# Kernel tuning notes

Measured on AMD Instinct MI355X. Metric: run time of the kernel, lower is better.

## Reference

```python
import jax, jax.numpy as jnp
import numpy as np

B, T, D = 2, 2048, 1024
H, HD = 16, 32
INNER = H * HD
FF = 4 * D
KT, KP = 3, 15


def _layernorm(x, g, b, eps=1e-5):
    mu = jnp.mean(x, axis=-1, keepdims=True)
    var = jnp.var(x, axis=-1, keepdims=True)
    return (x - mu) * jax.lax.rsqrt(var + eps) * g + b


def _causal_dwconv(x, w, b):
    # x: (b,t,d), w: (d,1,k) depthwise kernel; causal left-pad of k-1
    k = w.shape[-1]
    xc = jnp.transpose(x, (0, 2, 1))  # (b,d,t)
    xp = jnp.pad(xc, ((0, 0), (0, 0), (k - 1, 0)))
    y = jax.lax.conv_general_dilated(
        xp, w, window_strides=(1,), padding='VALID',
        feature_group_count=x.shape[-1],
        dimension_numbers=('NCH', 'OIH', 'NCH'))
    return jnp.transpose(y + b[None, :, None], (0, 2, 1))


def _causal_linear_attention(q, k, v, mask):
    # q,k,v: (b,t,h,d); mask: (b,t)
    m = mask[:, :, None, None]
    q = (jax.nn.elu(q) + 1.0) * m
    k = (jax.nn.elu(k) + 1.0) * m
    v = v * m
    kv = jnp.einsum('bthd,bthe->bthde', k, v)
    kv_prefix = jnp.cumsum(kv, axis=1)          # (b,t,h,d,e) large intermediate
    k_prefix = jnp.cumsum(k, axis=1)
    num = jnp.einsum('bthd,bthde->bthe', q, kv_prefix)
    den = jnp.sum(q * k_prefix, axis=-1, keepdims=True)
    return (num / (den + 1e-6)) * m


def setup_inputs() -> dict:
    key = jax.random.key(0)
    ks = jax.random.split(key, 10)
    w = lambda i, shape: jax.random.normal(ks[i], shape, jnp.float32) * 0.02
    return {
        'inputs': jax.random.normal(ks[0], (B, T, D), jnp.float32),
        'mask': jnp.ones((B, T), jnp.float32),
        'ln1_g': jnp.ones((D,), jnp.float32), 'ln1_b': jnp.zeros((D,), jnp.float32),
        'W_in': w(1, (D, D + 3 * INNER)), 'b_in': jnp.zeros((D + 3 * INNER,), jnp.float32),
        'W_c': w(2, (INNER, D)), 'b_c': jnp.zeros((D,), jnp.float32),
        'w_t': w(3, (D, 1, KT)), 'b_t': jnp.zeros((D,), jnp.float32),
        'w_p': w(4, (D, 1, KP)), 'b_p': jnp.zeros((D,), jnp.float32),
        'W_mix': w(5, (3 * D, D)), 'b_mix': jnp.zeros((D,), jnp.float32),
        'ln2_g': jnp.ones((D,), jnp.float32), 'ln2_b': jnp.zeros((D,), jnp.float32),
        'W1': w(6, (D, FF)), 'b1': jnp.zeros((FF,), jnp.float32),
        'W2': w(7, (FF, D)), 'b2': jnp.zeros((D,), jnp.float32),
    }


def reference(inputs, mask, ln1_g, ln1_b, W_in, b_in, W_c, b_c, w_t, b_t,
              w_p, b_p, W_mix, b_mix, ln2_g, ln2_b, W1, b1, W2, b2):
    residual = inputs
    normed = _layernorm(inputs, ln1_g, ln1_b)
    proj = normed @ W_in + b_in
    gate, q, k, v = jnp.split(proj, [D, D + INNER, D + 2 * INNER], axis=-1)
    b, t, _ = inputs.shape
    q = q.reshape(b, t, H, HD)
    k = k.reshape(b, t, H, HD)
    v = v.reshape(b, t, H, HD)
    content = _causal_linear_attention(q, k, v, mask).reshape(b, t, INNER)
    content = content @ W_c + b_c
    temporal = _causal_dwconv(normed, w_t, b_t)
    positional = _causal_dwconv(normed, w_p, b_p)
    mixed = jnp.concatenate((content, temporal, positional), axis=-1) @ W_mix + b_mix
    mask_f = mask[:, :, None]
    out = residual + jax.nn.sigmoid(gate) * mixed  # dropout=0.0 -> identity
    out = out * mask_f
    h = _layernorm(out, ln2_g, ln2_b)
    ffn = jax.nn.gelu(h @ W1 + b1, approximate=False) @ W2 + b2
    out = out + ffn
    return out * mask_f
```

## Files before the change

kernel.cpp:

```cpp
#include <hip/hip_runtime.h>
#include <math.h>

#define BB 2
#define TT 2048
#define DD 1024
#define HH 16
#define INNERD 512
#define FFD 4096
#define NPROJ 2560
#define CATD2 2560
#define MROWS (BB*TT)
#define CHUNK 64
#define NCH (TT/CHUNK)
#define BH 32

typedef __bf16 bf16;
typedef __attribute__((ext_vector_type(8))) __bf16 bf16x8;
typedef __attribute__((ext_vector_type(4))) __bf16 bf16x4;
typedef __attribute__((ext_vector_type(4))) float f32x4;

struct Part4 { void* p0; void* p1; void* p2; void* p3; };

__global__ __launch_bounds__(256) void prep_fused(
    const float* __restrict__ inputs, const float* __restrict__ ln1_g,
    const float* __restrict__ ln1_b, bf16* __restrict__ normed,
    const float* __restrict__ W_in,  bf16* __restrict__ wt_in,
    const float* __restrict__ W_mix, bf16* __restrict__ wt_m0,
    bf16* __restrict__ wt_comb,
    const float* __restrict__ W1,    bf16* __restrict__ wt1,
    const float* __restrict__ W2,    bf16* __restrict__ wt2,
    const float* __restrict__ W_c,   bf16* __restrict__ wc_b,
    const float* __restrict__ b_c,
    const float* __restrict__ b_mix, float* __restrict__ bmix2)
{
    int blk = blockIdx.x, tid = threadIdx.x;
    if (blk < 16) {
        int nl = tid & 63, jg = tid >> 6;
        int n = blk * 64 + nl;
        int j0 = jg * 256;
        float acc = 0.f;
        #pragma unroll 8
        for (int j = 0; j < 256; j++)
            acc = fmaf(b_c[j0 + j], W_mix[(size_t)(j0 + j) * DD + n], acc);
        __shared__ float red[4][64];
        red[jg][nl] = acc;
        __syncthreads();
        if (jg == 0)
            bmix2[n] = b_mix[n] + red[0][nl] + red[1][nl] + red[2][nl] + red[3][nl];
        return;
    }
    if (blk < 528) {
        int id = (blk - 16) * 256 + tid;
        f32x4 v = ((const f32x4*)W_c)[id];
        bf16x4 o;
        #pragma unroll
        for (int q = 0; q < 4; q++) o[q] = (bf16)v[q];
        ((bf16x4*)wc_b)[id] = o;
        return;
    }
    if (blk < 528 + MROWS) {
        int row = blk - 528;
        f32x4 xv = ((const f32x4*)(inputs + (size_t)row * DD))[tid];
        float s = xv[0] + xv[1] + xv[2] + xv[3];
        float s2 = xv[0]*xv[0] + xv[1]*xv[1] + xv[2]*xv[2] + xv[3]*xv[3];
        #pragma unroll
        for (int off = 32; off > 0; off >>= 1) {
            s  += __shfl_xor(s,  off, 64);
            s2 += __shfl_xor(s2, off, 64);
        }
        __shared__ float rs[4], rs2[4];
        int wid = tid >> 6;
        if ((tid & 63) == 0) { rs[wid] = s; rs2[wid] = s2; }
        __syncthreads();
        s  = rs[0] + rs[1] + rs[2] + rs[3];
        s2 = rs2[0] + rs2[1] + rs2[2] + rs2[3];
        float mean = s * (1.0f / DD);
        float var  = s2 * (1.0f / DD) - mean * mean;
        float rstd = rsqrtf(var + 1e-5f);
        f32x4 gv = ((const f32x4*)ln1_g)[tid];
        f32x4 bv = ((const f32x4*)ln1_b)[tid];
        bf16x4 o;
        #pragma unroll
        for (int q = 0; q < 4; q++)
            o[q] = (bf16)((xv[q] - mean) * rstd * gv[q] + bv[q]);
        ((bf16x4*)(normed + (size_t)row * DD))[tid] = o;
        return;
    }
    int tb = blk - (528 + MROWS);
    const float* W; bf16* Wt = nullptr; int Kd, Nd; bool is_mix = false;
    if      (tb < 2560)  {             W = W_in;  Wt = wt_in;  Kd = 1024; Nd = 2560; }
    else if (tb < 5632)  { tb -= 2560; W = W_mix;              Kd = 3072; Nd = 1024; is_mix = true; }
    else if (tb < 9728)  { tb -= 5632; W = W1;    Wt = wt1;    Kd = 1024; Nd = 4096; }
    else                 { tb -= 9728; W = W2;    Wt = wt2;    Kd = 4096; Nd = 1024; }
    int ntx = Nd >> 5;
    int nb = (tb % ntx) * 32, kb = (tb / ntx) * 32;
    int ldW = Kd, kw = kb;
    if (is_mix) {
        if (kb < 1024) { Wt = wt_m0;   ldW = 1024;  kw = kb; }
        else           { Wt = wt_comb; ldW = CATD2; kw = kb - 512; }
    }
    __shared__ float t[32][33];
    int tx = tid & 7, ty = tid >> 3;
    f32x4 v = *(const f32x4*)(W + (size_t)(kb + ty) * Nd + nb + tx * 4);
    #pragma unroll
    for (int q = 0; q < 4; q++) t[ty][tx * 4 + q] = v[q];
    __syncthreads();
    bf16x4 o;
    #pragma unroll
    for (int q = 0; q < 4; q++) o[q] = (bf16)t[tx * 4 + q][ty];
    *(bf16x4*)(Wt + (size_t)(nb + ty) * ldW + kw + tx * 4) = o;
}

template<int EPI>
__global__ __launch_bounds__(256, 4) void gemm_mfma(
    const bf16* __restrict__ A,  int lda,
    const bf16* __restrict__ Bt, int ldb,
    const float* __restrict__ bias,
    bf16* __restrict__ Cb, int ldc,
    int K, Part4 part)
{
    __shared__ bf16 As[128 * 64];
    __shared__ bf16 Bs[128 * 64];
    const int tid  = threadIdx.x;
    const int wave = tid >> 6, lane = tid & 63;
    const int m0 = blockIdx.x * 128, n0 = blockIdx.y * 128;
    const int koff = blockIdx.z * K;
    A  += koff;
    Bt += koff;
    const int wr = wave >> 1, wc = wave & 1;
    const int lrow = lane >> 2;
    const int lcol = (lane & 3) * 8;
    const int fm = lane & 15;
    const int fk = (lane >> 4) * 8;

    f32x4 acc[4][4];
    #pragma unroll
    for (int i = 0; i < 4; i++)
        #pragma unroll
        for (int j = 0; j < 4; j++)
            acc[i][j] = (f32x4){0.f, 0.f, 0.f, 0.f};

    for (int k0 = 0; k0 < K; k0 += 64) {
        #pragma unroll
        for (int r = 0; r < 4; r++) {
            int c  = r * 4 + wave;
            int rc = c >> 1, kh = c & 1;
            const bf16* ga = A  + (size_t)(m0 + rc * 16 + lrow) * lda + k0 + kh * 32 + lcol;
            const bf16* gb = Bt + (size_t)(n0 + rc * 16 + lrow) * ldb + k0 + kh * 32 + lcol;
            __builtin_amdgcn_global_load_lds(
                (const __attribute__((address_space(1))) void*)ga,
                (__attribute__((address_space(3))) void*)(As + c * 512), 16, 0, 0);
            __builtin_amdgcn_global_load_lds(
                (const __attribute__((address_space(1))) void*)gb,
                (__attribute__((address_space(3))) void*)(Bs + c * 512), 16, 0, 0);
        }
        __syncthreads();
        #pragma unroll
        for (int ks = 0; ks < 2; ks++) {
            bf16x8 af[4], bfv[4];
            #pragma unroll
            for (int i = 0; i < 4; i++)
                af[i] = *(const bf16x8*)(As + (wr * 4 + i) * 1024 + ks * 512 + fm * 32 + fk);
            #pragma unroll
            for (int j = 0; j < 4; j++)
                bfv[j] = *(const bf16x8*)(Bs + (wc * 4 + j) * 1024 + ks * 512 + fm * 32 + fk);
            #pragma unroll
            for (int i = 0; i < 4; i++)
                #pragma unroll
                for (int j = 0; j < 4; j++)
                    acc[i][j] = __builtin_amdgcn_mfma_f32_16x16x32_bf16(
                        af[i], bfv[j], acc[i][j], 0, 0, 0);
        }
        __syncthreads();
    }

    void* psel = nullptr;
    if constexpr (EPI == 4) {
        int z = blockIdx.z;
        psel = (z == 0) ? part.p0 : (z == 1) ? part.p1 : (z == 2) ? part.p2 : part.p3;
    }

    #pragma unroll
    for (int i = 0; i < 4; i++) {
        int mbase = m0 + wr * 64 + i * 16 + (lane >> 4) * 4;
        #pragma unroll
        for (int j = 0; j < 4; j++) {
            int col = n0 + wc * 64 + j * 16 + (lane & 15);
            float bv = 0.f;
            if constexpr (EPI == 0 || EPI == 1) bv = bias[col];
            #pragma unroll
            for (int r = 0; r < 4; r++) {
                int row = mbase + r;
                float v = acc[i][j][r] + bv;
                if constexpr (EPI == 0) {
                    Cb[(size_t)row * ldc + col] = (bf16)v;
                } else if constexpr (EPI == 1) {
                    float z2 = v * (1.5957691f + 0.07135502f * v * v);
                    v = v / (1.0f + __expf(-z2));
                    Cb[(size_t)row * ldc + col] = (bf16)v;
                } else {
                    ((bf16*)psel)[(size_t)row * DD + col] = (bf16)v;
                }
            }
        }
    }
}

__global__ __launch_bounds__(256, 4) void gemm_proj2(
    const bf16* __restrict__ normed, const bf16* __restrict__ wt_in,
    const float* __restrict__ bias,  bf16* __restrict__ proj,
    const bf16* __restrict__ wt_m0,  const bf16* __restrict__ wc_b,
    bf16* __restrict__ wt_comb)
{
    __shared__ bf16 As[128 * 64];
    __shared__ bf16 Bs[128 * 64];
    const int tid  = threadIdx.x;
    const int wave = tid >> 6, lane = tid & 63;
    const bool second = (blockIdx.y == 20);
    const bf16* A  = second ? wt_m0 : normed;
    const bf16* Bt = second ? wc_b  : wt_in;
    bf16* Cb       = second ? wt_comb : proj;
    const int m0 = second ? ((blockIdx.x >> 2) * 128) : (blockIdx.x * 128);
    const int n0 = second ? ((blockIdx.x & 3) * 128)  : (blockIdx.y * 128);
    const int wr = wave >> 1, wc = wave & 1;
    const int lrow = lane >> 2;
    const int lcol = (lane & 3) * 8;
    const int fm = lane & 15;
    const int fk = (lane >> 4) * 8;

    f32x4 acc[4][4];
    #pragma unroll
    for (int i = 0; i < 4; i++)
        #pragma unroll
        for (int j = 0; j < 4; j++)
            acc[i][j] = (f32x4){0.f, 0.f, 0.f, 0.f};

    for (int k0 = 0; k0 < DD; k0 += 64) {
        #pragma unroll
        for (int r = 0; r < 4; r++) {
            int c  = r * 4 + wave;
            int rc = c >> 1, kh = c & 1;
            const bf16* ga = A  + (size_t)(m0 + rc * 16 + lrow) * DD + k0 + kh * 32 + lcol;
            const bf16* gb = Bt + (size_t)(n0 + rc * 16 + lrow) * DD + k0 + kh * 32 + lcol;
            __builtin_amdgcn_global_load_lds(
                (const __attribute__((address_space(1))) void*)ga,
                (__attribute__((address_space(3))) void*)(As + c * 512), 16, 0, 0);
            __builtin_amdgcn_global_load_lds(
                (const __attribute__((address_space(1))) void*)gb,
                (__attribute__((address_space(3))) void*)(Bs + c * 512), 16, 0, 0);
        }
        __syncthreads();
        #pragma unroll
        for (int ks = 0; ks < 2; ks++) {
            bf16x8 af[4], bfv[4];
            #pragma unroll
            for (int i = 0; i < 4; i++)
                af[i] = *(const bf16x8*)(As + (wr * 4 + i) * 1024 + ks * 512 + fm * 32 + fk);
            #pragma unroll
            for (int j = 0; j < 4; j++)
                bfv[j] = *(const bf16x8*)(Bs + (wc * 4 + j) * 1024 + ks * 512 + fm * 32 + fk);
            #pragma unroll
            for (int i = 0; i < 4; i++)
                #pragma unroll
                for (int j = 0; j < 4; j++)
                    acc[i][j] = __builtin_amdgcn_mfma_f32_16x16x32_bf16(
                        af[i], bfv[j], acc[i][j], 0, 0, 0);
        }
        __syncthreads();
    }

    #pragma unroll
    for (int i = 0; i < 4; i++) {
        int mbase = m0 + wr * 64 + i * 16 + (lane >> 4) * 4;
        #pragma unroll
        for (int j = 0; j < 4; j++) {
            int col = n0 + wc * 64 + j * 16 + (lane & 15);
            float bv = second ? 0.f : bias[col];
            #pragma unroll
            for (int r = 0; r < 4; r++) {
                int row = mbase + r;
                Cb[(size_t)row * CATD2 + col] = (bf16)(acc[i][j][r] + bv);
            }
        }
    }
}

__global__ __launch_bounds__(256) void epi_mix_ln2(
    const bf16* __restrict__ P0, const bf16* __restrict__ P1,
    const float* __restrict__ bias,
    const bf16* __restrict__ proj, const float* __restrict__ res,
    const float* __restrict__ mask,
    const float* __restrict__ g2, const float* __restrict__ b2v,
    float* __restrict__ out1, bf16* __restrict__ hbuf)
{
    int row = blockIdx.x, tid = threadIdx.x;
    float m = mask[row];
    size_t off = (size_t)row * DD + tid * 4;
    bf16x4 s0 = *(const bf16x4*)(P0 + off);
    bf16x4 s1 = *(const bf16x4*)(P1 + off);
    f32x4 bv = ((const f32x4*)bias)[tid];
    bf16x4 g4 = *(const bf16x4*)(proj + (size_t)row * NPROJ + tid * 4);
    f32x4 rv = ((const f32x4*)(res + (size_t)row * DD))[tid];
    f32x4 v;
    #pragma unroll
    for (int q = 0; q < 4; q++) {
        float sg = 1.0f / (1.0f + __expf(-(float)g4[q]));
        float sv = (float)s0[q] + (float)s1[q] + bv[q];
        v[q] = (rv[q] + sg * sv) * m;
    }
    ((f32x4*)(out1 + (size_t)row * DD))[tid] = v;
    float s = v[0] + v[1] + v[2] + v[3];
    float s2 = v[0]*v[0] + v[1]*v[1] + v[2]*v[2] + v[3]*v[3];
    #pragma unroll
    for (int off2 = 32; off2 > 0; off2 >>= 1) {
        s  += __shfl_xor(s,  off2, 64);
        s2 += __shfl_xor(s2, off2, 64);
    }
    __shared__ float rs[4], rs2[4];
    int wid = tid >> 6;
    if ((tid & 63) == 0) { rs[wid] = s; rs2[wid] = s2; }
    __syncthreads();
    s  = rs[0] + rs[1] + rs[2] + rs[3];
    s2 = rs2[0] + rs2[1] + rs2[2] + rs2[3];
    float mean = s * (1.0f / DD);
    float var  = s2 * (1.0f / DD) - mean * mean;
    float rstd = rsqrtf(var + 1e-5f);
    f32x4 gg = ((const f32x4*)g2)[tid];
    f32x4 bb = ((const f32x4*)b2v)[tid];
    bf16x4 h;
    #pragma unroll
    for (int q = 0; q < 4; q++)
        h[q] = (bf16)((v[q] - mean) * rstd * gg[q] + bb[q]);
    ((bf16x4*)(hbuf + (size_t)row * DD))[tid] = h;
}

__global__ __launch_bounds__(256) void epi_w2(
    float* __restrict__ d_out, const float* __restrict__ out1,
    const bf16* __restrict__ P0, const bf16* __restrict__ P1,
    const bf16* __restrict__ P2, const bf16* __restrict__ P3,
    const float* __restrict__ bias, const float* __restrict__ mask)
{
    int id = blockIdx.x * 256 + threadIdx.x;
    int row = id >> 8;
    float m = mask[row];
    bf16x4 a0 = ((const bf16x4*)P0)[id];
    bf16x4 a1 = ((const bf16x4*)P1)[id];
    bf16x4 a2 = ((const bf16x4*)P2)[id];
    bf16x4 a3 = ((const bf16x4*)P3)[id];
    f32x4 r = ((const f32x4*)out1)[id];
    f32x4 b = ((const f32x4*)bias)[id & 255];
    f32x4 o;
    #pragma unroll
    for (int q = 0; q < 4; q++) {
        float sv = (float)a0[q] + (float)a1[q] + (float)a2[q] + (float)a3[q];
        o[q] = (r[q] + sv + b[q]) * m;
    }
    ((f32x4*)d_out)[id] = o;
}

__device__ __forceinline__ float phi_f(float x) {
    return x > 0.f ? x + 1.f : __expf(x);
}

__global__ __launch_bounds__(256) void mid_fused(
    const bf16* __restrict__ x,
    const float* __restrict__ w_t, const float* __restrict__ b_t,
    const float* __restrict__ w_p, const float* __restrict__ b_p,
    bf16* __restrict__ cat,
    const bf16* __restrict__ proj, const float* __restrict__ mask,
    float* __restrict__ kvsum, float* __restrict__ kssum)
{
    __shared__ float s_ks[2][CHUNK][32], s_vs[2][CHUNK][32];
    int blk = blockIdx.x, tid = threadIdx.x;
    if (blk < 1024) {
        int id = blk * 256 + tid;
        int cg = id & 127, rp = id >> 7;
        int c0 = cg * 8;
        int row0 = rp * 2;
        int t0 = row0 & (TT - 1);
        bf16x8 xw[16];
        #pragma unroll
        for (int j = 0; j < 16; j++) {
            int t = t0 - 14 + j;
            if (t >= 0)
                xw[j] = *(const bf16x8*)(x + (size_t)(row0 - 14 + j) * DD + c0);
            else
                #pragma unroll
                for (int q = 0; q < 8; q++) xw[j][q] = (bf16)0.f;
        }
        float y15[2][8], y3[2][8];
        #pragma unroll
        for (int q = 0; q < 8; q++) {
            float bp = b_p[c0 + q], bt = b_t[c0 + q];
            y15[0][q] = bp; y15[1][q] = bp;
            y3[0][q] = bt;  y3[1][q] = bt;
        }
        #pragma unroll
        for (int i = 0; i < 15; i++) {
            float wp[8];
            #pragma unroll
            for (int q = 0; q < 8; q++) wp[q] = w_p[(c0 + q) * 15 + i];
            #pragma unroll
            for (int rr = 0; rr < 2; rr++)
                #pragma unroll
                for (int q = 0; q < 8; q++)
                    y15[rr][q] = fmaf(wp[q], (float)xw[rr + i][q], y15[rr][q]);
        }
        #pragma unroll
        for (int i = 0; i < 3; i++) {
            float wt[8];
            #pragma unroll
            for (int q = 0; q < 8; q++) wt[q] = w_t[(c0 + q) * 3 + i];
            #pragma unroll
            for (int rr = 0; rr < 2; rr++)
                #pragma unroll
                for (int q = 0; q < 8; q++)
                    y3[rr][q] = fmaf(wt[q], (float)xw[rr + 12 + i][q], y3[rr][q]);
        }
        #pragma unroll
        for (int rr = 0; rr < 2; rr++) {
            bf16x8 o3, o15;
            #pragma unroll
            for (int q = 0; q < 8; q++) { o3[q] = (bf16)y3[rr][q]; o15[q] = (bf16)y15[rr][q]; }
            *(bf16x8*)(cat + (size_t)(row0 + rr) * CATD2 + 512 + c0)  = o3;
            *(bf16x8*)(cat + (size_t)(row0 + rr) * CATD2 + 1536 + c0) = o15;
        }
        return;
    }
    int w = tid >> 6;
    if (w >= 2) return;
    int lane = tid & 63;
    int ci = (blk - 1024) * 2 + w;
    int c  = ci & (NCH - 1);
    int bh = ci >> 5;
    int b  = bh >> 4, hh = bh & (HH - 1);
    float (*ks)[32] = s_ks[w];
    float (*vs)[32] = s_vs[w];
    int row0 = b * TT + c * CHUNK;
    {
        int row = row0 + lane;
        float m = mask[row];
        const bf16* kp = proj + (size_t)row * NPROJ + DD + INNERD + hh * 32;
        const bf16* vp = kp + INNERD;
        #pragma unroll
        for (int s = 0; s < 4; s++) {
            bf16x8 k8 = *(const bf16x8*)(kp + s * 8);
            bf16x8 v8 = *(const bf16x8*)(vp + s * 8);
            #pragma unroll
            for (int q = 0; q < 8; q++) {
                ks[lane][s * 8 + q] = phi_f((float)k8[q]) * m;
                vs[lane][s * 8 + q] = (float)v8[q] * m;
            }
        }
    }
    int e = lane & 31, d0 = (lane >> 5) * 16;
    float kv[16], ksl[16];
    #pragma unroll
    for (int j = 0; j < 16; j++) { kv[j] = 0.f; ksl[j] = 0.f; }
    for (int t = 0; t < CHUNK; t++) {
        float ve = vs[t][e];
        f32x4 kr[4];
        #pragma unroll
        for (int s = 0; s < 4; s++) kr[s] = *(const f32x4*)&ks[t][d0 + s * 4];
        #pragma unroll
        for (int j = 0; j < 16; j++) {
            float kval = kr[j >> 2][j & 3];
            kv[j] = fmaf(kval, ve, kv[j]);
            ksl[j] += kval;
        }
    }
    size_t base = (size_t)ci * 1024;
    #pragma unroll
    for (int j = 0; j < 16; j++)
        kvsum[base + (size_t)(d0 + j) * 32 + e] = kv[j];
    if (e == 0) {
        #pragma unroll
        for (int j = 0; j < 16; j++)
            kssum[ci * 32 + d0 + j] = ksl[j];
    }
}

__global__ __launch_bounds__(256) void attn_prefix(
    const float* __restrict__ kvsum, const float* __restrict__ kssum,
    float* __restrict__ kvpref, float* __restrict__ kspref)
{
    int blk = blockIdx.x, tid = threadIdx.x;
    if (blk < 128) {
        int bh = blk >> 2;
        int de = (blk & 3) * 256 + tid;
        float run = 0.f;
        for (int c = 0; c < NCH; c++) {
            size_t a = (size_t)(bh * NCH + c) * 1024 + de;
            kvpref[a] = run;
            run += kvsum[a];
        }
        return;
    }
    int id = (blk - 128) * 256 + tid;
    int bh = id >> 5, d = id & 31;
    float r = 0.f;
    for (int c = 0; c < NCH; c++) {
        int a = (bh * NCH + c) * 32 + d;
        kspref[a] = r;
        r += kssum[a];
    }
}

__global__ __launch_bounds__(64) void attn_scan(
    const bf16* __restrict__ proj, const float* __restrict__ mask,
    const float* __restrict__ kvpref, const float* __restrict__ kspref,
    bf16* __restrict__ cat)
{
    int blk = blockIdx.x;
    int c  = blk & (NCH - 1);
    int bh = blk >> 5;
    int b  = bh >> 4, hh = bh & (HH - 1);
    int lane = threadIdx.x;
    __shared__ float qs[CHUNK][32], ks[CHUNK][32], vs[CHUNK][32];
    __shared__ float ms[CHUNK];
    int row0 = b * TT + c * CHUNK;
    {
        int row = row0 + lane;
        float m = mask[row];
        ms[lane] = m;
        const bf16* qp = proj + (size_t)row * NPROJ + DD + hh * 32;
        const bf16* kp = qp + INNERD;
        const bf16* vp = kp + INNERD;
        #pragma unroll
        for (int s = 0; s < 4; s++) {
            bf16x8 q8 = *(const bf16x8*)(qp + s * 8);
            bf16x8 k8 = *(const bf16x8*)(kp + s * 8);
            bf16x8 v8 = *(const bf16x8*)(vp + s * 8);
            #pragma unroll
            for (int q = 0; q < 8; q++) {
                qs[lane][s * 8 + q] = phi_f((float)q8[q]) * m;
                ks[lane][s * 8 + q] = phi_f((float)k8[q]) * m;
                vs[lane][s * 8 + q] = (float)v8[q] * m;
            }
        }
    }
    int e = lane & 31, d0 = (lane >> 5) * 16;
    float kv[16], ksl[16];
    size_t base = (size_t)blk * 1024;
    #pragma unroll
    for (int j = 0; j < 16; j++) kv[j] = kvpref[base + (size_t)(d0 + j) * 32 + e];
    #pragma unroll
    for (int j = 0; j < 16; j++) ksl[j] = kspref[blk * 32 + d0 + j];
    __syncthreads();
    for (int t = 0; t < CHUNK; t++) {
        float ve = vs[t][e];
        f32x4 kr[4], qr[4];
        #pragma unroll
        for (int s = 0; s < 4; s++) kr[s] = *(const f32x4*)&ks[t][d0 + s * 4];
        #pragma unroll
        for (int s = 0; s < 4; s++) qr[s] = *(const f32x4*)&qs[t][d0 + s * 4];
        float num0 = 0.f, num1 = 0.f, den0 = 0.f, den1 = 0.f;
        #pragma unroll
        for (int j = 0; j < 16; j++) {
            float kval = kr[j >> 2][j & 3], qval = qr[j >> 2][j & 3];
            kv[j]  = fmaf(kval, ve, kv[j]);
            ksl[j] += kval;
            if (j & 1) { num1 = fmaf(qval, kv[j], num1); den1 = fmaf(qval, ksl[j], den1); }
            else       { num0 = fmaf(qval, kv[j], num0); den0 = fmaf(qval, ksl[j], den0); }
        }
        float num = num0 + num1, den = den0 + den1;
        num += __shfl_xor(num, 32, 64);
        den += __shfl_xor(den, 32, 64);
        if (lane < 32)
            cat[(size_t)(row0 + t) * CATD2 + hh * 32 + e] =
                (bf16)(num / (den + 1e-6f) * ms[t]);
    }
}

extern "C" void kernel_launch(void* const* d_in, const int* in_sizes, int n_in,
                              void* d_out, int out_size, void* d_ws, size_t ws_size,
                              hipStream_t stream)
{
    const float* inputs = (const float*)d_in[0];
    const float* mask   = (const float*)d_in[1];
    const float* ln1_g  = (const float*)d_in[2];
    const float* ln1_b  = (const float*)d_in[3];
    const float* W_in   = (const float*)d_in[4];
    const float* b_in   = (const float*)d_in[5];
    const float* W_c    = (const float*)d_in[6];
    const float* b_c    = (const float*)d_in[7];
    const float* w_t    = (const float*)d_in[8];
    const float* b_t    = (const float*)d_in[9];
    const float* w_p    = (const float*)d_in[10];
    const float* b_p    = (const float*)d_in[11];
    const float* W_mix  = (const float*)d_in[12];
    const float* b_mix  = (const float*)d_in[13];
    const float* ln2_g  = (const float*)d_in[14];
    const float* ln2_b  = (const float*)d_in[15];
    const float* W1     = (const float*)d_in[16];
    const float* b1     = (const float*)d_in[17];
    const float* W2     = (const float*)d_in[18];
    const float* b2     = (const float*)d_in[19];
    float* out = (float*)d_out;

    char* p = (char*)d_ws;
    bf16* normed = (bf16*)p;  p += (size_t)MROWS * DD * 2;
    bf16* proj   = (bf16*)p;  p += (size_t)MROWS * NPROJ * 2;
    bf16* cat    = (bf16*)p;  p += (size_t)MROWS * CATD2 * 2;
    float* out1  = (float*)p; p += (size_t)MROWS * DD * 4;
    bf16* hbuf   = (bf16*)p;  p += (size_t)MROWS * DD * 2;
    bf16* wt_in  = (bf16*)p;  p += (size_t)NPROJ * DD * 2;
    bf16* wt_m0  = (bf16*)p;  p += (size_t)DD * DD * 2;
    bf16* wt_comb= (bf16*)p;  p += (size_t)DD * CATD2 * 2;
    bf16* wt1    = (bf16*)p;  p += (size_t)FFD * DD * 2;
    bf16* wt2    = (bf16*)p;  p += (size_t)DD * FFD * 2;
    bf16* wc_b   = (bf16*)p;  p += (size_t)INNERD * DD * 2;
    float* bmix2 = (float*)p; p += (size_t)DD * 4;
    bf16* ffn1   = (bf16*)d_ws;
    float* kvsum = out1;
    float* kvpref= kvsum  + (size_t)BH * NCH * 1024;
    float* kssum = kvpref + (size_t)BH * NCH * 1024;
    float* kspref= kssum  + (size_t)BH * NCH * 32;
    bf16*  m_p0  = (bf16*)d_out;
    bf16*  m_p1  = (bf16*)d_out + (size_t)MROWS * DD;
    bf16*  w2_p0 = (bf16*)((char*)cat + ((size_t)4  << 20));
    bf16*  w2_p1 = (bf16*)((char*)cat + ((size_t)12 << 20));
    bf16*  w2_p2 = wt1;
    bf16*  w2_p3 = hbuf;

    prep_fused<<<16 + 512 + MROWS + 13824, 256, 0, stream>>>(
        inputs, ln1_g, ln1_b, normed,
        W_in, wt_in, W_mix, wt_m0, wt_comb, W1, wt1, W2, wt2,
        W_c, wc_b, b_c, b_mix, bmix2);
    gemm_proj2<<<dim3(MROWS/128, NPROJ/128 + 1), 256, 0, stream>>>(
        normed, wt_in, b_in, proj, wt_m0, wc_b, wt_comb);
    mid_fused<<<1024 + 512, 256, 0, stream>>>(
        normed, w_t, b_t, w_p, b_p, cat, proj, mask, kvsum, kssum);
    attn_prefix<<<132, 256, 0, stream>>>(kvsum, kssum, kvpref, kspref);
    attn_scan  <<<BH * NCH, 64, 0, stream>>>(proj, mask, kvpref, kspref, cat);
    gemm_mfma<4><<<dim3(MROWS/128, DD/128, 2), 256, 0, stream>>>(
        cat, CATD2, wt_comb, CATD2, nullptr, nullptr, DD, CATD2 / 2,
        Part4{m_p0, m_p1, nullptr, nullptr});
    epi_mix_ln2<<<MROWS, 256, 0, stream>>>(m_p0, m_p1, bmix2, proj, inputs,
                                           mask, ln2_g, ln2_b, out1, hbuf);
    gemm_mfma<1><<<dim3(MROWS/128, FFD/128), 256, 0, stream>>>(
        hbuf, DD, wt1, DD, b1, ffn1, FFD, DD, Part4{});
    gemm_mfma<4><<<dim3(MROWS/128, DD/128, 4), 256, 0, stream>>>(
        ffn1, FFD, wt2, FFD, nullptr, nullptr, DD, FFD / 4,
        Part4{w2_p0, w2_p1, w2_p2, w2_p3});
    epi_w2<<<MROWS * DD / 4 / 256, 256, 0, stream>>>(out, out1, w2_p0, w2_p1,
                                                     w2_p2, w2_p3, b2, mask);
}
```

Measured before the change: 380.5 us.

## Add 256x256-tile 8-wave MFMA GEMM with interleaved LDS prefetch for FFN

Introduces a new GEMM kernel with 256x256 block tiles, 512 threads and double-buffered LDS staged via direct global-to-LDS loads. The loads are interleaved between MFMA phases with explicit waitcnt, barriers and setprio. Both FFN GEMMs (W1 with GELU, split-K W2) switch to this kernel. The goal is more data reuse per block and better overlap of memory with MFMA. The trade-off is fewer blocks: 256 for W1 and 256 for W2 split-K, on a GPU with 256 CUs. It also uses 128KB of LDS and more registers, which limits occupancy.

```diff
diff --git a/kernel.cpp b/kernel.cpp
--- a/kernel.cpp
+++ b/kernel.cpp
@@ -186,6 +186,153 @@
         #pragma unroll
         for (int j = 0; j < 4; j++) {
             int col = n0 + wc * 64 + j * 16 + (lane & 15);
+            float bv = 0.f;
+            if constexpr (EPI == 0 || EPI == 1) bv = bias[col];
+            #pragma unroll
+            for (int r = 0; r < 4; r++) {
+                int row = mbase + r;
+                float v = acc[i][j][r] + bv;
+                if constexpr (EPI == 0) {
+                    Cb[(size_t)row * ldc + col] = (bf16)v;
+                } else if constexpr (EPI == 1) {
+                    float z2 = v * (1.5957691f + 0.07135502f * v * v);
+                    v = v / (1.0f + __expf(-z2));
+                    Cb[(size_t)row * ldc + col] = (bf16)v;
+                } else {
+                    ((bf16*)psel)[(size_t)row * DD + col] = (bf16)v;
+                }
+            }
+        }
+    }
+}
+
+__device__ __forceinline__ void stage_half256(
+    const bf16* __restrict__ src, int ld, int k0, int rowbase,
+    bf16* ldsHalf, int wave, int sr, int sc)
+{
+    #pragma unroll
+    for (int i = 0; i < 2; i++) {
+        int s  = wave * 2 + i;
+        int rg = s >> 1, cg = s & 1;
+        const bf16* g = src + (size_t)(rowbase + rg * 16 + sr) * ld + k0 + cg * 32 + sc;
+        __builtin_amdgcn_global_load_lds(
+            (const __attribute__((address_space(1))) void*)g,
+            (__attribute__((address_space(3))) void*)(ldsHalf + s * 512), 16, 0, 0);
+    }
+}
+
+template<int EPI>
+__global__ __launch_bounds__(512) void gemm256(
+    const bf16* __restrict__ A,  int lda,
+    const bf16* __restrict__ Bt, int ldb,
+    const float* __restrict__ bias,
+    bf16* __restrict__ Cb, int ldc,
+    int K, Part4 part)
+{
+    __shared__ bf16 sA[2 * 2 * 8192];
+    __shared__ bf16 sB[2 * 2 * 8192];
+    const int tid  = threadIdx.x;
+    const int wave = tid >> 6, lane = tid & 63;
+    const int m0 = blockIdx.x * 256, n0 = blockIdx.y * 256;
+    A  += (size_t)m0 * lda + (size_t)blockIdx.z * K;
+    Bt += (size_t)n0 * ldb + (size_t)blockIdx.z * K;
+    const int wr = wave >> 2, wc = wave & 3;
+    const int wcl = wc & 1;
+    const int sr = lane >> 2;
+    const int sc = ((lane & 3) * 8) ^ ((sr & 8) ? 16 : 0);
+    const int fm = lane & 15;
+    const int fro = ((fm * 32) + ((lane >> 4) * 8)) ^ ((fm & 8) ? 16 : 0);
+
+    f32x4 acc[8][4];
+    #pragma unroll
+    for (int i = 0; i < 8; i++)
+        #pragma unroll
+        for (int j = 0; j < 4; j++)
+            acc[i][j] = (f32x4){0.f, 0.f, 0.f, 0.f};
+
+    const int NT = K >> 6;
+    stage_half256(Bt, ldb, 0, 0,   sB,          wave, sr, sc);
+    stage_half256(Bt, ldb, 0, 128, sB + 8192,   wave, sr, sc);
+    stage_half256(A,  lda, 0, 0,   sA,          wave, sr, sc);
+    stage_half256(A,  lda, 0, 128, sA + 8192,   wave, sr, sc);
+    if (NT > 1) {
+        stage_half256(Bt, ldb, 64, 0,   sB + 16384, wave, sr, sc);
+        stage_half256(Bt, ldb, 64, 128, sB + 24576, wave, sr, sc);
+        stage_half256(A,  lda, 64, 0,   sA + 16384, wave, sr, sc);
+        asm volatile("s_waitcnt vmcnt(6)" ::: "memory");
+    } else {
+        asm volatile("s_waitcnt vmcnt(0)" ::: "memory");
+    }
+    __builtin_amdgcn_s_barrier();
+
+    for (int t = 0; t < NT; t++) {
+        const int cur = t & 1, nxt = cur ^ 1;
+        const bf16* pA = sA + (cur * 2 + wr) * 8192;
+        const bf16* pB = sB + (cur * 2 + (wc >> 1)) * 8192;
+        bf16* sAn1 = sA + (nxt * 2 + 1) * 8192;
+        bf16* sBc0 = sB + (cur * 2 + 0) * 8192;
+        bf16* sBc1 = sB + (cur * 2 + 1) * 8192;
+        bf16* sAc0 = sA + (cur * 2 + 0) * 8192;
+        const int kt1 = (t + 1) << 6, kt2 = (t + 2) << 6;
+        bf16x8 bq[4][2];
+        #pragma unroll
+        for (int p = 0; p < 4; p++) {
+            bf16x8 aq[2][2];
+            if (p == 0) {
+                #pragma unroll
+                for (int j = 0; j < 4; j++)
+                    #pragma unroll
+                    for (int ks = 0; ks < 2; ks++)
+                        bq[j][ks] = *(const bf16x8*)(pB + ((wcl * 4 + j) * 2 + ks) * 512 + fro);
+            }
+            #pragma unroll
+            for (int ii = 0; ii < 2; ii++)
+                #pragma unroll
+                for (int ks = 0; ks < 2; ks++)
+                    aq[ii][ks] = *(const bf16x8*)(pA + (((p * 2 + ii) * 2) + ks) * 512 + fro);
+            if (p == 0) {
+                if (t + 1 < NT) stage_half256(A, lda, kt1, 128, sAn1, wave, sr, sc);
+                asm volatile("s_waitcnt lgkmcnt(8)" ::: "memory");
+            } else if (p == 1) {
+                if (t + 2 < NT) stage_half256(Bt, ldb, kt2, 0, sBc0, wave, sr, sc);
+            } else if (p == 2) {
+                if (t + 2 < NT) stage_half256(Bt, ldb, kt2, 128, sBc1, wave, sr, sc);
+            }
+            __builtin_amdgcn_s_barrier();
+            asm volatile("s_waitcnt lgkmcnt(0)" ::: "memory");
+            __builtin_amdgcn_sched_barrier(0);
+            __builtin_amdgcn_s_setprio(1);
+            #pragma unroll
+            for (int ii = 0; ii < 2; ii++)
+                #pragma unroll
+                for (int j = 0; j < 4; j++)
+                    #pragma unroll
+                    for (int ks = 0; ks < 2; ks++)
+                        acc[p * 2 + ii][j] = __builtin_amdgcn_mfma_f32_16x16x32_bf16(
+                            aq[ii][ks], bq[j][ks], acc[p * 2 + ii][j], 0, 0, 0);
+            __builtin_amdgcn_s_setprio(0);
+            __builtin_amdgcn_s_barrier();
+        }
+        if (t + 2 < NT) stage_half256(A, lda, kt2, 0, sAc0, wave, sr, sc);
+        if (t + 1 < NT) {
+            if (t + 2 < NT) asm volatile("s_waitcnt vmcnt(6)" ::: "memory");
+            else            asm volatile("s_waitcnt vmcnt(0)" ::: "memory");
+            __builtin_amdgcn_s_barrier();
+        }
+    }
+
+    void* psel = nullptr;
+    if constexpr (EPI == 4) {
+        int z = blockIdx.z;
+        psel = (z == 0) ? part.p0 : (z == 1) ? part.p1 : (z == 2) ? part.p2 : part.p3;
+    }
+
+    #pragma unroll
+    for (int i = 0; i < 8; i++) {
+        int mbase = m0 + wr * 128 + i * 16 + (lane >> 4) * 4;
+        #pragma unroll
+        for (int j = 0; j < 4; j++) {
+            int col = n0 + wc * 64 + j * 16 + fm;
             float bv = 0.f;
             if constexpr (EPI == 0 || EPI == 1) bv = bias[col];
             #pragma unroll
@@ -638,9 +785,9 @@
         Part4{m_p0, m_p1, nullptr, nullptr});
     epi_mix_ln2<<<MROWS, 256, 0, stream>>>(m_p0, m_p1, bmix2, proj, inputs,
                                            mask, ln2_g, ln2_b, out1, hbuf);
-    gemm_mfma<1><<<dim3(MROWS/128, FFD/128), 256, 0, stream>>>(
+    gemm256<1><<<dim3(MROWS/256, FFD/256), 512, 0, stream>>>(
         hbuf, DD, wt1, DD, b1, ffn1, FFD, DD, Part4{});
-    gemm_mfma<4><<<dim3(MROWS/128, DD/128, 4), 256, 0, stream>>>(
+    gemm256<4><<<dim3(MROWS/256, DD/256, 4), 512, 0, stream>>>(
         ffn1, FFD, wt2, FFD, nullptr, nullptr, DD, FFD / 4,
         Part4{w2_p0, w2_p1, w2_p2, w2_p3});
     epi_w2<<<MROWS * DD / 4 / 256, 256, 0, stream>>>(out, out1, w2_p0, w2_p1,
```

Result: no change. 387.5 us (+1.8%).
